# Kernel optimization log

Hardware: AMD Instinct MI355X
Metric: run time of the kernel (lower is better)

## Reference

```python
import jax, jax.numpy as jnp
import numpy as np

B, S, D = 4, 2048, 1024
E = 8
H = int(D * 2.5)  # 2560


def setup_inputs() -> dict:
    key = jax.random.key(0)
    ks = jax.random.split(key, 6)
    scale = 0.02
    x = jax.random.normal(ks[0], (B, S, D), dtype=jnp.float32)
    Wr = jax.random.normal(ks[1], (E, D), dtype=jnp.float32) * scale   # router: logits = x @ Wr.T
    Wg = jax.random.normal(ks[2], (E, H, D), dtype=jnp.float32) * scale  # gate proj per expert
    Wu = jax.random.normal(ks[3], (E, H, D), dtype=jnp.float32) * scale  # up proj per expert
    Wd = jax.random.normal(ks[4], (E, D, H), dtype=jnp.float32) * scale  # down proj per expert
    return {"x": x, "Wr": Wr, "Wg": Wg, "Wu": Wu, "Wd": Wd, "top_k": 2}


def reference(x, Wr, Wg, Wu, Wd, top_k):
    num_experts = Wg.shape[0]
    logits = jnp.einsum('bsd,ed->bse', x, Wr)              # [B,S,E]
    probs = jax.nn.softmax(logits, axis=-1)
    k = min(top_k, num_experts)
    topv, topi = jax.lax.top_k(probs, k)                   # [B,S,k]
    out = jnp.zeros_like(x)
    for ei in range(num_experts):
        mask = jnp.any(topi == ei, axis=-1)                # [B,S] bool
        h = jax.nn.silu(jnp.einsum('bsd,hd->bsh', x, Wg[ei])) \
            * jnp.einsum('bsd,hd->bsh', x, Wu[ei])         # [B,S,H]
        ex = jnp.einsum('bsh,dh->bsd', h, Wd[ei])          # [B,S,D]
        w = (probs[..., ei] * mask.astype(x.dtype))[..., None]
        out = out + ex * w
    return (out, logits, probs, topi)
```

## Files before the change

kernel.cpp:

```cpp
#include <hip/hip_runtime.h>

#define T_TOK 8192
#define DD    1024
#define EE    8
#define HH    2560
#define PAIR_CAP (T_TOK*2 + 128)
#define MT_MAX 64
#define NT1   (HH/64)
#define NT2   (DD/128)

typedef __attribute__((ext_vector_type(8))) short bf16x8;
typedef __attribute__((ext_vector_type(4))) float f32x4;

__device__ __forceinline__ unsigned short f2b(float f) {
  union { float f; unsigned u; } v; v.f = f;
  unsigned r = v.u + 0x7FFFu + ((v.u >> 16) & 1u);
  return (unsigned short)(r >> 16);
}

__device__ __forceinline__ void async16(const void* g, void* l) {
  __builtin_amdgcn_global_load_lds(
      (const __attribute__((address_space(1))) unsigned int*)(unsigned long long)g,
      (__attribute__((address_space(3))) unsigned int*)l,
      16, 0, 0);
}

__global__ void zero_ints(int* a, int n) {
  int i = threadIdx.x;
  if (i < n) a[i] = 0;
}

__global__ void conv_bf16(const float* __restrict__ s, unsigned short* __restrict__ d, int n4) {
  int i = blockIdx.x * blockDim.x + threadIdx.x;
  if (i >= n4) return;
  float4 v = ((const float4*)s)[i];
  ushort4 o;
  o.x = f2b(v.x); o.y = f2b(v.y); o.z = f2b(v.z); o.w = f2b(v.w);
  ((ushort4*)d)[i] = o;
}

__global__ __launch_bounds__(256) void router(
    const float* __restrict__ x, const float* __restrict__ Wr,
    float* __restrict__ o_logits, float* __restrict__ o_probs, float* __restrict__ o_topi,
    int* __restrict__ top_e, float* __restrict__ top_p, int* __restrict__ counts)
{
  __shared__ float sWr[EE * DD];
  int tid = threadIdx.x;
  const float4* w4 = (const float4*)Wr;
  float4* s4 = (float4*)sWr;
  for (int i = tid; i < EE * DD / 4; i += 256) s4[i] = w4[i];
  __syncthreads();

  int wv = tid >> 6, lane = tid & 63;
  int t = blockIdx.x * 4 + wv;
  const float* xt = x + (size_t)t * DD;

  float acc[EE];
#pragma unroll
  for (int e = 0; e < EE; e++) acc[e] = 0.f;
  for (int d = lane; d < DD; d += 64) {
    float xv = xt[d];
#pragma unroll
    for (int e = 0; e < EE; e++) acc[e] += xv * sWr[e * DD + d];
  }
#pragma unroll
  for (int e = 0; e < EE; e++) {
#pragma unroll
    for (int off = 32; off; off >>= 1) acc[e] += __shfl_down(acc[e], off);
  }
  if (lane == 0) {
    float mx = acc[0];
#pragma unroll
    for (int e = 1; e < EE; e++) mx = fmaxf(mx, acc[e]);
    float p[EE]; float sum = 0.f;
#pragma unroll
    for (int e = 0; e < EE; e++) { p[e] = __expf(acc[e] - mx); sum += p[e]; }
    float inv = 1.f / sum;
#pragma unroll
    for (int e = 0; e < EE; e++) {
      p[e] *= inv;
      o_logits[(size_t)t * EE + e] = acc[e];
      o_probs [(size_t)t * EE + e] = p[e];
    }
    int i0 = 0;
#pragma unroll
    for (int e = 1; e < EE; e++) if (p[e] > p[i0]) i0 = e;
    int i1 = (i0 == 0) ? 1 : 0;
#pragma unroll
    for (int e = 0; e < EE; e++) if (e != i0 && p[e] > p[i1]) i1 = e;

    o_topi[t * 2 + 0] = (float)i0;
    o_topi[t * 2 + 1] = (float)i1;
    top_e[t * 2 + 0] = i0; top_e[t * 2 + 1] = i1;
    top_p[t * 2 + 0] = p[i0]; top_p[t * 2 + 1] = p[i1];
    atomicAdd(&counts[i0], 1);
    atomicAdd(&counts[i1], 1);
  }
}

__global__ void mk_offsets(const int* __restrict__ counts, int* __restrict__ offsets,
                           int* __restrict__ cursors) {
  if (threadIdx.x == 0) {
    int s = 0;
    for (int e = 0; e < EE; e++) { offsets[e] = s; s += counts[e]; }
  }
  if (threadIdx.x < EE) cursors[threadIdx.x] = 0;
}

__global__ void scatter(const int* __restrict__ top_e,
                        const int* __restrict__ offsets, int* __restrict__ cursors,
                        int* __restrict__ list, int* __restrict__ slot) {
  int t = blockIdx.x * blockDim.x + threadIdx.x;
  if (t >= T_TOK) return;
#pragma unroll
  for (int k = 0; k < 2; k++) {
    int e = top_e[t * 2 + k];
    int pos = atomicAdd(&cursors[e], 1);
    int dst = offsets[e] + pos;
    list[dst] = t;
    slot[t * 2 + k] = dst;
  }
}

__global__ __launch_bounds__(256) void gemm_gateup(
    const unsigned short* __restrict__ xb,
    const unsigned short* __restrict__ Wgb,
    const unsigned short* __restrict__ Wub,
    const int* __restrict__ list, const int* __restrict__ offsets,
    const int* __restrict__ counts,
    unsigned short* __restrict__ hbuf)
{
  int bx = blockIdx.x;
  int e = bx / (MT_MAX * NT1);
  int rem = bx - e * (MT_MAX * NT1);
  int mt = rem / NT1;
  int nt = rem - mt * NT1;
  int n_e = counts[e];
  if (mt * 128 >= n_e) return;
  int off_e = offsets[e];

  __shared__ unsigned short sA [128 * 64];
  __shared__ unsigned short sBg[ 64 * 64];
  __shared__ unsigned short sBu[ 64 * 64];

  int tid = threadIdx.x, wv = tid >> 6, lane = tid & 63;
  const unsigned short* wg_e = Wgb + (size_t)e * HH * DD;
  const unsigned short* wu_e = Wub + (size_t)e * HH * DD;

  size_t aBase[4];
#pragma unroll
  for (int i = 0; i < 4; i++) {
    int c = i * 256 + tid;
    int r = c >> 3, j = c & 7;
    int jj = j ^ (r & 7);
    int idx = mt * 128 + r;
    if (idx >= n_e) idx = n_e - 1;
    int tok = list[off_e + idx];
    aBase[i] = (size_t)tok * DD + (size_t)(jj * 8);
  }
  size_t bBase[2];
#pragma unroll
  for (int i = 0; i < 2; i++) {
    int c = i * 256 + tid;
    int r = c >> 3, j = c & 7;
    int jj = j ^ (r & 7);
    bBase[i] = (size_t)(nt * 64 + r) * DD + (size_t)(jj * 8);
  }

  f32x4 accg[4][2] = {};
  f32x4 accu[4][2] = {};
  int wm = (wv >> 1) * 64, wn = (wv & 1) * 32;

  for (int k0 = 0; k0 < DD; k0 += 64) {
    __syncthreads();
#pragma unroll
    for (int i = 0; i < 4; i++)
      async16(xb + aBase[i] + k0, sA + (size_t)(i * 256 + wv * 64) * 8);
#pragma unroll
    for (int i = 0; i < 2; i++) {
      async16(wg_e + bBase[i] + k0, sBg + (size_t)(i * 256 + wv * 64) * 8);
      async16(wu_e + bBase[i] + k0, sBu + (size_t)(i * 256 + wv * 64) * 8);
    }
    __syncthreads();

#pragma unroll
    for (int ks = 0; ks < 2; ks++) {
      bf16x8 af[4], bg[2], bu[2];
#pragma unroll
      for (int fi = 0; fi < 4; fi++) {
        int r = wm + fi * 16 + (lane & 15);
        int ch = (ks * 4 + (lane >> 4)) ^ (r & 7);
        af[fi] = *(const bf16x8*)&sA[r * 64 + ch * 8];
      }
#pragma unroll
      for (int fj = 0; fj < 2; fj++) {
        int r = wn + fj * 16 + (lane & 15);
        int ch = (ks * 4 + (lane >> 4)) ^ (r & 7);
        bg[fj] = *(const bf16x8*)&sBg[r * 64 + ch * 8];
        bu[fj] = *(const bf16x8*)&sBu[r * 64 + ch * 8];
      }
#pragma unroll
      for (int fi = 0; fi < 4; fi++)
#pragma unroll
        for (int fj = 0; fj < 2; fj++) {
          accg[fi][fj] = __builtin_amdgcn_mfma_f32_16x16x32_bf16(af[fi], bg[fj], accg[fi][fj], 0, 0, 0);
          accu[fi][fj] = __builtin_amdgcn_mfma_f32_16x16x32_bf16(af[fi], bu[fj], accu[fi][fj], 0, 0, 0);
        }
    }
  }

#pragma unroll
  for (int fi = 0; fi < 4; fi++) {
    int mBase = mt * 128 + wm + fi * 16 + ((lane >> 4) << 2);
#pragma unroll
    for (int fj = 0; fj < 2; fj++) {
      int col = nt * 64 + wn + fj * 16 + (lane & 15);
#pragma unroll
      for (int r = 0; r < 4; r++) {
        int m = mBase + r;
        if (m < n_e) {
          float g = accg[fi][fj][r];
          float u = accu[fi][fj][r];
          float hv = g / (1.f + __expf(-g)) * u;
          hbuf[(size_t)(off_e + m) * HH + col] = f2b(hv);
        }
      }
    }
  }
}

__global__ __launch_bounds__(256) void gemm_down(
    const unsigned short* __restrict__ hbuf,
    const unsigned short* __restrict__ Wdb,
    const int* __restrict__ offsets,
    const int* __restrict__ counts,
    float* __restrict__ tmp)
{
  int bx = blockIdx.x;
  int e = bx / (MT_MAX * NT2);
  int rem = bx - e * (MT_MAX * NT2);
  int mt = rem / NT2;
  int nt = rem - mt * NT2;
  int n_e = counts[e];
  if (mt * 128 >= n_e) return;
  int off_e = offsets[e];

  __shared__ unsigned short sA[128 * 64];
  __shared__ unsigned short sB[128 * 64];
  int tid = threadIdx.x, wv = tid >> 6, lane = tid & 63;
  const unsigned short* wd_e = Wdb + (size_t)e * DD * HH;

  size_t aBase[4], bBase[4];
#pragma unroll
  for (int i = 0; i < 4; i++) {
    int c = i * 256 + tid;
    int r = c >> 3, j = c & 7;
    int jj = j ^ (r & 7);
    aBase[i] = (size_t)(off_e + mt * 128 + r) * HH + (size_t)(jj * 8);
    bBase[i] = (size_t)(nt * 128 + r) * HH + (size_t)(jj * 8);
  }

  f32x4 acc[4][4] = {};
  int wm = (wv >> 1) * 64, wn = (wv & 1) * 64;

  for (int k0 = 0; k0 < HH; k0 += 64) {
    __syncthreads();
#pragma unroll
    for (int i = 0; i < 4; i++) {
      async16(hbuf + aBase[i] + k0, sA + (size_t)(i * 256 + wv * 64) * 8);
      async16(wd_e + bBase[i] + k0, sB + (size_t)(i * 256 + wv * 64) * 8);
    }
    __syncthreads();

#pragma unroll
    for (int ks = 0; ks < 2; ks++) {
      bf16x8 af[4], bf[4];
#pragma unroll
      for (int f = 0; f < 4; f++) {
        int ra = wm + f * 16 + (lane & 15);
        int ca = (ks * 4 + (lane >> 4)) ^ (ra & 7);
        af[f] = *(const bf16x8*)&sA[ra * 64 + ca * 8];
        int rb = wn + f * 16 + (lane & 15);
        int cb = (ks * 4 + (lane >> 4)) ^ (rb & 7);
        bf[f] = *(const bf16x8*)&sB[rb * 64 + cb * 8];
      }
#pragma unroll
      for (int fi = 0; fi < 4; fi++)
#pragma unroll
        for (int fj = 0; fj < 4; fj++)
          acc[fi][fj] = __builtin_amdgcn_mfma_f32_16x16x32_bf16(af[fi], bf[fj], acc[fi][fj], 0, 0, 0);
    }
  }

#pragma unroll
  for (int fi = 0; fi < 4; fi++) {
    int mBase = mt * 128 + wm + fi * 16 + ((lane >> 4) << 2);
#pragma unroll
    for (int r = 0; r < 4; r++) {
      int m = mBase + r;
      if (m < n_e) {
        float* orow = tmp + (size_t)(off_e + m) * DD + nt * 128 + wn;
#pragma unroll
        for (int fj = 0; fj < 4; fj++)
          orow[fj * 16 + (lane & 15)] = acc[fi][fj][r];
      }
    }
  }
}

__global__ __launch_bounds__(256) void combine(
    const float* __restrict__ tmp, const int* __restrict__ slot,
    const float* __restrict__ top_p, float* __restrict__ out)
{
  int t = blockIdx.x, d = threadIdx.x;
  int s0 = slot[t * 2 + 0], s1 = slot[t * 2 + 1];
  float p0 = top_p[t * 2 + 0], p1 = top_p[t * 2 + 1];
  float4 a = ((const float4*)(tmp + (size_t)s0 * DD))[d];
  float4 b = ((const float4*)(tmp + (size_t)s1 * DD))[d];
  float4 o;
  o.x = p0 * a.x + p1 * b.x;
  o.y = p0 * a.y + p1 * b.y;
  o.z = p0 * a.z + p1 * b.z;
  o.w = p0 * a.w + p1 * b.w;
  ((float4*)(out + (size_t)t * DD))[d] = o;
}

extern "C" void kernel_launch(void* const* d_in, const int* in_sizes, int n_in,
                              void* d_out, int out_size, void* d_ws, size_t ws_size,
                              hipStream_t stream) {
  const float* x  = (const float*)d_in[0];
  const float* Wr = (const float*)d_in[1];
  const float* Wg = (const float*)d_in[2];
  const float* Wu = (const float*)d_in[3];
  const float* Wd = (const float*)d_in[4];

  float* out      = (float*)d_out;
  float* o_logits = out + (size_t)T_TOK * DD;
  float* o_probs  = o_logits + (size_t)T_TOK * EE;
  float* o_topi   = o_probs + (size_t)T_TOK * EE;

  char* w = (char*)d_ws;
  auto alloc = [&](size_t bytes) {
    char* p = w;
    w += (bytes + 255) & ~(size_t)255;
    return p;
  };
  unsigned short* Wgb = (unsigned short*)alloc((size_t)EE * HH * DD * 2);
  unsigned short* Wub = (unsigned short*)alloc((size_t)EE * HH * DD * 2);
  unsigned short* Wdb = (unsigned short*)alloc((size_t)EE * DD * HH * 2);
  unsigned short* xb  = (unsigned short*)alloc((size_t)T_TOK * DD * 2);
  unsigned short* hb  = (unsigned short*)alloc((size_t)PAIR_CAP * HH * 2);
  int*   top_e   = (int*)  alloc((size_t)T_TOK * 2 * 4);
  float* top_p   = (float*)alloc((size_t)T_TOK * 2 * 4);
  int*   counts  = (int*)  alloc(64);
  int*   offsets = (int*)  alloc(64);
  int*   cursors = (int*)  alloc(64);
  int*   list    = (int*)  alloc((size_t)PAIR_CAP * 4);
  int*   slot    = (int*)  alloc((size_t)T_TOK * 2 * 4);

  float* tmp = (float*)Wgb;

  zero_ints<<<1, 64, 0, stream>>>(counts, EE);
  {
    int nw4 = EE * HH * DD / 4;
    conv_bf16<<<(nw4 + 255) / 256, 256, 0, stream>>>(Wg, Wgb, nw4);
    conv_bf16<<<(nw4 + 255) / 256, 256, 0, stream>>>(Wu, Wub, nw4);
    conv_bf16<<<(nw4 + 255) / 256, 256, 0, stream>>>(Wd, Wdb, nw4);
    int nx4 = T_TOK * DD / 4;
    conv_bf16<<<(nx4 + 255) / 256, 256, 0, stream>>>(x, xb, nx4);
  }
  router<<<T_TOK / 4, 256, 0, stream>>>(x, Wr, o_logits, o_probs, o_topi, top_e, top_p, counts);
  mk_offsets<<<1, 64, 0, stream>>>(counts, offsets, cursors);
  scatter<<<T_TOK / 256, 256, 0, stream>>>(top_e, offsets, cursors, list, slot);
  gemm_gateup<<<EE * MT_MAX * NT1, 256, 0, stream>>>(xb, Wgb, Wub, list, offsets, counts, hb);
  gemm_down<<<EE * MT_MAX * NT2, 256, 0, stream>>>(hb, Wdb, offsets, counts, tmp);
  combine<<<T_TOK, 256, 0, stream>>>(tmp, slot, top_p, out);
}
```

Baseline: 942.6 us.

## Double-buffer LDS in both expert GEMMs and fuse x bf16 conversion into router

```diff
diff --git a/kernel.cpp b/kernel.cpp
--- a/kernel.cpp
+++ b/kernel.cpp
@@ -41,6 +41,7 @@
 
 __global__ __launch_bounds__(256) void router(
     const float* __restrict__ x, const float* __restrict__ Wr,
+    unsigned short* __restrict__ xb,
     float* __restrict__ o_logits, float* __restrict__ o_probs, float* __restrict__ o_topi,
     int* __restrict__ top_e, float* __restrict__ top_p, int* __restrict__ counts)
 {
@@ -53,15 +54,24 @@
 
   int wv = tid >> 6, lane = tid & 63;
   int t = blockIdx.x * 4 + wv;
-  const float* xt = x + (size_t)t * DD;
+  const float4* xt4 = (const float4*)(x + (size_t)t * DD);
+  ushort4* xbt = (ushort4*)(xb + (size_t)t * DD);
 
   float acc[EE];
 #pragma unroll
   for (int e = 0; e < EE; e++) acc[e] = 0.f;
-  for (int d = lane; d < DD; d += 64) {
-    float xv = xt[d];
-#pragma unroll
-    for (int e = 0; e < EE; e++) acc[e] += xv * sWr[e * DD + d];
+#pragma unroll
+  for (int p = 0; p < 4; p++) {
+    float4 v = xt4[p * 64 + lane];
+    ushort4 o;
+    o.x = f2b(v.x); o.y = f2b(v.y); o.z = f2b(v.z); o.w = f2b(v.w);
+    xbt[p * 64 + lane] = o;
+    int d = (p * 64 + lane) * 4;
+#pragma unroll
+    for (int e = 0; e < EE; e++) {
+      const float* wr = &sWr[e * DD + d];
+      acc[e] += v.x * wr[0] + v.y * wr[1] + v.z * wr[2] + v.w * wr[3];
+    }
   }
 #pragma unroll
   for (int e = 0; e < EE; e++) {
@@ -139,74 +149,72 @@
   if (mt * 128 >= n_e) return;
   int off_e = offsets[e];
 
-  __shared__ unsigned short sA [128 * 64];
-  __shared__ unsigned short sBg[ 64 * 64];
-  __shared__ unsigned short sBu[ 64 * 64];
+  __shared__ unsigned short sA [2][128 * 32];
+  __shared__ unsigned short sBg[2][ 64 * 32];
+  __shared__ unsigned short sBu[2][ 64 * 32];
 
   int tid = threadIdx.x, wv = tid >> 6, lane = tid & 63;
   const unsigned short* wg_e = Wgb + (size_t)e * HH * DD;
   const unsigned short* wu_e = Wub + (size_t)e * HH * DD;
 
-  size_t aBase[4];
-#pragma unroll
-  for (int i = 0; i < 4; i++) {
+  size_t aBase[2];
+#pragma unroll
+  for (int i = 0; i < 2; i++) {
     int c = i * 256 + tid;
-    int r = c >> 3, j = c & 7;
-    int jj = j ^ (r & 7);
+    int r = c >> 2, j = c & 3;
+    int jj = j ^ ((r >> 1) & 3);
     int idx = mt * 128 + r;
     if (idx >= n_e) idx = n_e - 1;
     int tok = list[off_e + idx];
     aBase[i] = (size_t)tok * DD + (size_t)(jj * 8);
   }
-  size_t bBase[2];
-#pragma unroll
-  for (int i = 0; i < 2; i++) {
-    int c = i * 256 + tid;
-    int r = c >> 3, j = c & 7;
-    int jj = j ^ (r & 7);
-    bBase[i] = (size_t)(nt * 64 + r) * DD + (size_t)(jj * 8);
+  size_t bBase;
+  {
+    int r = tid >> 2, j = tid & 3;
+    int jj = j ^ ((r >> 1) & 3);
+    bBase = (size_t)(nt * 64 + r) * DD + (size_t)(jj * 8);
   }
 
   f32x4 accg[4][2] = {};
   f32x4 accu[4][2] = {};
   int wm = (wv >> 1) * 64, wn = (wv & 1) * 32;
 
-  for (int k0 = 0; k0 < DD; k0 += 64) {
+  auto stage = [&](int b, int k0) {
+    async16(xb  + aBase[0] + k0, &sA [b][(      wv * 64) * 8]);
+    async16(xb  + aBase[1] + k0, &sA [b][(256 + wv * 64) * 8]);
+    async16(wg_e + bBase   + k0, &sBg[b][(      wv * 64) * 8]);
+    async16(wu_e + bBase   + k0, &sBu[b][(      wv * 64) * 8]);
+  };
+
+  stage(0, 0);
+  int cur = 0;
+  int q = lane >> 4;
+  for (int k0 = 0; k0 < DD; k0 += 32) {
     __syncthreads();
-#pragma unroll
-    for (int i = 0; i < 4; i++)
-      async16(xb + aBase[i] + k0, sA + (size_t)(i * 256 + wv * 64) * 8);
-#pragma unroll
-    for (int i = 0; i < 2; i++) {
-      async16(wg_e + bBase[i] + k0, sBg + (size_t)(i * 256 + wv * 64) * 8);
-      async16(wu_e + bBase[i] + k0, sBu + (size_t)(i * 256 + wv * 64) * 8);
-    }
-    __syncthreads();
-
-#pragma unroll
-    for (int ks = 0; ks < 2; ks++) {
-      bf16x8 af[4], bg[2], bu[2];
-#pragma unroll
-      for (int fi = 0; fi < 4; fi++) {
-        int r = wm + fi * 16 + (lane & 15);
-        int ch = (ks * 4 + (lane >> 4)) ^ (r & 7);
-        af[fi] = *(const bf16x8*)&sA[r * 64 + ch * 8];
+    if (k0 + 32 < DD) stage(cur ^ 1, k0 + 32);
+
+    bf16x8 af[4], bg[2], bu[2];
+#pragma unroll
+    for (int fi = 0; fi < 4; fi++) {
+      int r = wm + fi * 16 + (lane & 15);
+      int ch = q ^ ((r >> 1) & 3);
+      af[fi] = *(const bf16x8*)&sA[cur][r * 32 + ch * 8];
+    }
+#pragma unroll
+    for (int fj = 0; fj < 2; fj++) {
+      int r = wn + fj * 16 + (lane & 15);
+      int ch = q ^ ((r >> 1) & 3);
+      bg[fj] = *(const bf16x8*)&sBg[cur][r * 32 + ch * 8];
+      bu[fj] = *(const bf16x8*)&sBu[cur][r * 32 + ch * 8];
+    }
+#pragma unroll
+    for (int fi = 0; fi < 4; fi++)
+#pragma unroll
+      for (int fj = 0; fj < 2; fj++) {
+        accg[fi][fj] = __builtin_amdgcn_mfma_f32_16x16x32_bf16(af[fi], bg[fj], accg[fi][fj], 0, 0, 0);
+        accu[fi][fj] = __builtin_amdgcn_mfma_f32_16x16x32_bf16(af[fi], bu[fj], accu[fi][fj], 0, 0, 0);
       }
-#pragma unroll
-      for (int fj = 0; fj < 2; fj++) {
-        int r = wn + fj * 16 + (lane & 15);
-        int ch = (ks * 4 + (lane >> 4)) ^ (r & 7);
-        bg[fj] = *(const bf16x8*)&sBg[r * 64 + ch * 8];
-        bu[fj] = *(const bf16x8*)&sBu[r * 64 + ch * 8];
-      }
-#pragma unroll
-      for (int fi = 0; fi < 4; fi++)
-#pragma unroll
-        for (int fj = 0; fj < 2; fj++) {
-          accg[fi][fj] = __builtin_amdgcn_mfma_f32_16x16x32_bf16(af[fi], bg[fj], accg[fi][fj], 0, 0, 0);
-          accu[fi][fj] = __builtin_amdgcn_mfma_f32_16x16x32_bf16(af[fi], bu[fj], accu[fi][fj], 0, 0, 0);
-        }
-    }
+    cur ^= 1;
   }
 
 #pragma unroll
@@ -245,17 +253,17 @@
   if (mt * 128 >= n_e) return;
   int off_e = offsets[e];
 
-  __shared__ unsigned short sA[128 * 64];
-  __shared__ unsigned short sB[128 * 64];
+  __shared__ unsigned short sA[2][128 * 32];
+  __shared__ unsigned short sB[2][128 * 32];
   int tid = threadIdx.x, wv = tid >> 6, lane = tid & 63;
   const unsigned short* wd_e = Wdb + (size_t)e * DD * HH;
 
-  size_t aBase[4], bBase[4];
-#pragma unroll
-  for (int i = 0; i < 4; i++) {
+  size_t aBase[2], bBase[2];
+#pragma unroll
+  for (int i = 0; i < 2; i++) {
     int c = i * 256 + tid;
-    int r = c >> 3, j = c & 7;
-    int jj = j ^ (r & 7);
+    int r = c >> 2, j = c & 3;
+    int jj = j ^ ((r >> 1) & 3);
     aBase[i] = (size_t)(off_e + mt * 128 + r) * HH + (size_t)(jj * 8);
     bBase[i] = (size_t)(nt * 128 + r) * HH + (size_t)(jj * 8);
   }
@@ -263,33 +271,36 @@
   f32x4 acc[4][4] = {};
   int wm = (wv >> 1) * 64, wn = (wv & 1) * 64;
 
-  for (int k0 = 0; k0 < HH; k0 += 64) {
+  auto stage = [&](int b, int k0) {
+    async16(hbuf + aBase[0] + k0, &sA[b][(      wv * 64) * 8]);
+    async16(hbuf + aBase[1] + k0, &sA[b][(256 + wv * 64) * 8]);
+    async16(wd_e + bBase[0] + k0, &sB[b][(      wv * 64) * 8]);
+    async16(wd_e + bBase[1] + k0, &sB[b][(256 + wv * 64) * 8]);
+  };
+
+  stage(0, 0);
+  int cur = 0;
+  int q = lane >> 4;
+  for (int k0 = 0; k0 < HH; k0 += 32) {
     __syncthreads();
-#pragma unroll
-    for (int i = 0; i < 4; i++) {
-      async16(hbuf + aBase[i] + k0, sA + (size_t)(i * 256 + wv * 64) * 8);
-      async16(wd_e + bBase[i] + k0, sB + (size_t)(i * 256 + wv * 64) * 8);
-    }
-    __syncthreads();
-
-#pragma unroll
-    for (int ks = 0; ks < 2; ks++) {
-      bf16x8 af[4], bf[4];
-#pragma unroll
-      for (int f = 0; f < 4; f++) {
-        int ra = wm + f * 16 + (lane & 15);
-        int ca = (ks * 4 + (lane >> 4)) ^ (ra & 7);
-        af[f] = *(const bf16x8*)&sA[ra * 64 + ca * 8];
-        int rb = wn + f * 16 + (lane & 15);
-        int cb = (ks * 4 + (lane >> 4)) ^ (rb & 7);
-        bf[f] = *(const bf16x8*)&sB[rb * 64 + cb * 8];
-      }
-#pragma unroll
-      for (int fi = 0; fi < 4; fi++)
-#pragma unroll
-        for (int fj = 0; fj < 4; fj++)
-          acc[fi][fj] = __builtin_amdgcn_mfma_f32_16x16x32_bf16(af[fi], bf[fj], acc[fi][fj], 0, 0, 0);
-    }
+    if (k0 + 32 < HH) stage(cur ^ 1, k0 + 32);
+
+    bf16x8 af[4], bfr[4];
+#pragma unroll
+    for (int f = 0; f < 4; f++) {
+      int ra = wm + f * 16 + (lane & 15);
+      int ca = q ^ ((ra >> 1) & 3);
+      af[f] = *(const bf16x8*)&sA[cur][ra * 32 + ca * 8];
+      int rb = wn + f * 16 + (lane & 15);
+      int cb = q ^ ((rb >> 1) & 3);
+      bfr[f] = *(const bf16x8*)&sB[cur][rb * 32 + cb * 8];
+    }
+#pragma unroll
+    for (int fi = 0; fi < 4; fi++)
+#pragma unroll
+      for (int fj = 0; fj < 4; fj++)
+        acc[fi][fj] = __builtin_amdgcn_mfma_f32_16x16x32_bf16(af[fi], bfr[fj], acc[fi][fj], 0, 0, 0);
+    cur ^= 1;
   }
 
 #pragma unroll
@@ -366,10 +377,8 @@
     conv_bf16<<<(nw4 + 255) / 256, 256, 0, stream>>>(Wg, Wgb, nw4);
     conv_bf16<<<(nw4 + 255) / 256, 256, 0, stream>>>(Wu, Wub, nw4);
     conv_bf16<<<(nw4 + 255) / 256, 256, 0, stream>>>(Wd, Wdb, nw4);
-    int nx4 = T_TOK * DD / 4;
-    conv_bf16<<<(nx4 + 255) / 256, 256, 0, stream>>>(x, xb, nx4);
-  }
-  router<<<T_TOK / 4, 256, 0, stream>>>(x, Wr, o_logits, o_probs, o_topi, top_e, top_p, counts);
+  }
+  router<<<T_TOK / 4, 256, 0, stream>>>(x, Wr, xb, o_logits, o_probs, o_topi, top_e, top_p, counts);
   mk_offsets<<<1, 64, 0, stream>>>(counts, offsets, cursors);
   scatter<<<T_TOK / 256, 256, 0, stream>>>(top_e, offsets, cursors, list, slot);
   gemm_gateup<<<EE * MT_MAX * NT1, 256, 0, stream>>>(xb, Wgb, Wub, list, offsets, counts, hb);
```

New measurement: 983.0 us. 4.3% more time.
